# Performance work log

Measured on AMD Instinct MI355X. Metric: run time of the kernel, lower is better.

The kernel has to match this reference:

```python
import jax, jax.numpy as jnp
import numpy as np

G, P = 512, 128            # graphs, nodes per graph
NT, NL, NC = 120, 4, 4     # tracks/leptons/cells per graph (disjoint node targets)
W_NODE, W_BCE, W_F1 = 1.0, 1.0, 1.0  # config['loss weights']


def setup_inputs() -> dict:
    key = jax.random.key(0)
    ks = jax.random.split(key, 8)
    N = G * P
    T, L, C = G * NT, G * NL, G * NC
    E = G * P * P
    local = np.arange(P)[None, :] + (np.arange(G)[:, None] * P)  # [G,P] global node ids
    track_dst = jnp.asarray(local[:, :NT].ravel(), jnp.int32)
    lep_dst = jnp.asarray(local[:, NT:NT + NL].ravel(), jnp.int32)
    cell_dst = jnp.asarray(local[:, NT + NL:].ravel(), jnp.int32)
    ii, jj = np.meshgrid(np.arange(P), np.arange(P), indexing='ij')
    off = (np.arange(G) * P)[:, None, None]
    edge_src = jnp.asarray((off + ii[None]).reshape(-1), jnp.int32)
    edge_dst = jnp.asarray((off + jj[None]).reshape(-1), jnp.int32)
    edge_gid = jnp.asarray(np.repeat(np.arange(G), P * P), jnp.int32)
    node_gid = jnp.asarray(np.repeat(np.arange(G), P), jnp.int32)
    return {
        'node_prediction': jax.random.normal(ks[0], (N, 5), jnp.float32),
        'edge_prediction': jax.random.normal(ks[1], (E,), jnp.float32),
        'ce_weight': jnp.ones((5,), jnp.float32),
        'track_labels': jax.random.randint(ks[2], (T,), 0, 5, jnp.int32),
        'track_vtx': jax.random.randint(ks[3], (T,), 0, 10, jnp.int32),
        'lep_labels': jax.random.randint(ks[4], (L,), 0, 5, jnp.int32),
        'lep_vtx': jax.random.randint(ks[5], (L,), 0, 10, jnp.int32),
        'cell_labels': jax.random.randint(ks[6], (C,), 0, 5, jnp.int32),
        'cell_vtx': jax.random.randint(ks[7], (C,), 0, 10, jnp.int32),
        'track_dst': track_dst,
        'lep_dst': lep_dst,
        'cell_dst': cell_dst,
        'edge_src': edge_src,
        'edge_dst': edge_dst,
        'edge_gid': edge_gid,
        'node_gid': node_gid,
    }


def reference(node_prediction, edge_prediction, ce_weight,
              track_labels, track_vtx, lep_labels, lep_vtx, cell_labels, cell_vtx,
              track_dst, lep_dst, cell_dst, edge_src, edge_dst, edge_gid, node_gid):
    N = node_prediction.shape[0]

    def scatter(track_v, lep_v, cell_v):  # copy_src + sum over 3 edge types
        out = jnp.zeros((N,), jnp.int32)
        out = out.at[track_dst].add(track_v)
        out = out.at[lep_dst].add(lep_v)
        out = out.at[cell_dst].add(cell_v)
        return out

    node_labels = scatter(track_labels, lep_labels, cell_labels)
    node_vtx = scatter(track_vtx, lep_vtx, cell_vtx)

    # node CrossEntropyLoss (weight=[1]*5, ignore_index=-1, reduction='none')
    logp = jax.nn.log_softmax(node_prediction, axis=-1)
    valid = node_labels != -1
    lab = jnp.clip(node_labels, 0, 4)
    ce = -jnp.take_along_axis(logp, lab[:, None], axis=-1)[:, 0] * ce_weight[lab]
    ce = jnp.where(valid, ce, 0.0)
    node_loss = jax.ops.segment_sum(ce, node_gid, num_segments=G).mean()

    # edge weights (EdgeWeightFunction) and labels (EdgeLabelFunction)
    src_lab = node_labels[edge_src]
    dst_lab = node_labels[edge_dst]
    cond = ((dst_lab == 3) | (dst_lab == 2)) & ((src_lab == 3) | (src_lab == 2))
    w = jnp.where(cond, 2.0, 1.0).astype(jnp.float32)
    y = (node_vtx[edge_src] == node_vtx[edge_dst]).astype(jnp.float32)

    x = edge_prediction
    # BCEWithLogits: log(1+e^x) - x*y
    bce = (jnp.logaddexp(0.0, x) - x * y) * w
    e_cnt = jax.ops.segment_sum(jnp.ones_like(x), edge_gid, num_segments=G)
    edge_bce = (jax.ops.segment_sum(bce, edge_gid, num_segments=G) / e_cnt).mean()

    yh = jax.nn.sigmoid(x)
    tp = jax.ops.segment_sum(yh * y * w, edge_gid, num_segments=G)
    fn = jax.ops.segment_sum((1.0 - yh) * y * w, edge_gid, num_segments=G)
    fp = jax.ops.segment_sum(yh * (1.0 - y) * w, edge_gid, num_segments=G)
    edge_f1 = -(2.0 * tp / (2.0 * tp + fp + fn + 1e-10)).mean()

    loss = node_loss * W_NODE + edge_bce * W_BCE + edge_f1 * W_F1
    return loss
```

## Files before the change

kernel.cpp:

```cpp
#include <hip/hip_runtime.h>
#include <math.h>

#define NG     512
#define NP     128
#define NTRK   120
#define NLEP   4
#define NCEL   4
#define EPG    (NP * NP)
#define NTHREADS 1024
#define F4ITERS (EPG / (NTHREADS * 4))

__global__ __launch_bounds__(NTHREADS) void vfl_main(
    const float* __restrict__ node_pred,
    const float* __restrict__ edge_pred,
    const float* __restrict__ ce_weight,
    const int* __restrict__ track_labels, const int* __restrict__ track_vtx,
    const int* __restrict__ lep_labels,   const int* __restrict__ lep_vtx,
    const int* __restrict__ cell_labels,  const int* __restrict__ cell_vtx,
    float* __restrict__ gout)
{
    const int g = blockIdx.x;
    const int t = threadIdx.x;
    const int wv = t >> 6;
    const int ln = t & 63;

    __shared__ float s_edge[EPG];
    __shared__ int   s_pack[NP];
    __shared__ float s_red[16][4];
    __shared__ int   s_cnt[10][2];

    {
        const float* ep_base = edge_pred + (size_t)g * EPG;
        #pragma unroll
        for (int k = 0; k < 4; ++k) {
            const int c = (k << 4) + wv;
            const float* gsrc = ep_base + c * 256 + ln * 4;
            __builtin_amdgcn_global_load_lds(
                (const __attribute__((address_space(1))) void*)gsrc,
                (__attribute__((address_space(3))) void*)&s_edge[c * 256],
                16, 0, 0);
        }
    }

    if (t < 20) ((int*)s_cnt)[t] = 0;

    float ce = 0.0f;
    int vtx = 0, is23 = 0;
    if (t < NP) {
        int lab;
        if (t < NTRK) {
            lab = track_labels[g * NTRK + t];
            vtx = track_vtx  [g * NTRK + t];
        } else if (t < NTRK + NLEP) {
            const int u = t - NTRK;
            lab = lep_labels[g * NLEP + u];
            vtx = lep_vtx  [g * NLEP + u];
        } else {
            const int u = t - NTRK - NLEP;
            lab = cell_labels[g * NCEL + u];
            vtx = cell_vtx  [g * NCEL + u];
        }
        is23 = (lab == 2 || lab == 3) ? 1 : 0;
        s_pack[t] = (vtx & 0xff) | (is23 << 8);

        const float* np = node_pred + (size_t)(g * NP + t) * 5;
        const float x0 = np[0], x1 = np[1], x2 = np[2], x3 = np[3], x4 = np[4];
        const float m  = fmaxf(fmaxf(fmaxf(x0, x1), fmaxf(x2, x3)), x4);
        const float sm = __expf(x0 - m) + __expf(x1 - m) + __expf(x2 - m)
                       + __expf(x3 - m) + __expf(x4 - m);
        const float lse = m + __logf(sm);
        const float xl = (lab == 0) ? x0 : (lab == 1) ? x1 : (lab == 2) ? x2
                       : (lab == 3) ? x3 : x4;
        ce = (lse - xl) * ce_weight[lab];
    }

    asm volatile("s_waitcnt vmcnt(0)" ::: "memory");
    __syncthreads();

    if (t < NP) atomicAdd(&s_cnt[vtx][is23], 1);

    const int j0 = (t & 31) << 2;
    const int pj0 = s_pack[j0 + 0];
    const int pj1 = s_pack[j0 + 1];
    const int pj2 = s_pack[j0 + 2];
    const int pj3 = s_pack[j0 + 3];
    const int ibase = t >> 5;

    const float4* se4 = (const float4*)s_edge;

    float bce = 0.0f, swyh = 0.0f, tp = 0.0f;

    #pragma unroll
    for (int k = 0; k < F4ITERS; ++k) {
        const float4 v  = se4[k * NTHREADS + t];
        const int    pi = s_pack[ibase + k * 32];

        const float xs[4]  = { v.x, v.y, v.z, v.w };
        const int   pjs[4] = { pj0, pj1, pj2, pj3 };
        #pragma unroll
        for (int c = 0; c < 4; ++c) {
            const float x   = xs[c];
            const int   pjc = pjs[c];
            const bool  same = (((pi ^ pjc) & 0xff) == 0);
            const float w   = ((pi & pjc) & 0x100) ? 2.0f : 1.0f;
            const float wf  = same ? w : 0.0f;
            const float e  = __expf(-fabsf(x));
            const float t1 = 1.0f + e;
            const float r  = __builtin_amdgcn_rcpf(t1);
            const float sp = fmaxf(x, 0.0f) + __logf(t1);
            const float yh = (x >= 0.0f) ? r : (1.0f - r);
            bce  = fmaf(w,  sp, bce);
            bce  = fmaf(wf, -x, bce);
            swyh = fmaf(w,  yh, swyh);
            tp   = fmaf(wf, yh, tp);
        }
    }

    float vals[4] = { ce, bce, swyh, tp };
    #pragma unroll
    for (int i = 0; i < 4; ++i) {
        float x = vals[i];
        #pragma unroll
        for (int off = 32; off > 0; off >>= 1)
            x += __shfl_xor(x, off, 64);
        vals[i] = x;
    }
    if (ln == 0) {
        #pragma unroll
        for (int i = 0; i < 4; ++i) s_red[wv][i] = vals[i];
    }
    __syncthreads();

    if (t < 64) {
        float x[4];
        #pragma unroll
        for (int i = 0; i < 4; ++i)
            x[i] = (t < 16) ? s_red[t][i] : 0.0f;
        #pragma unroll
        for (int i = 0; i < 4; ++i) {
            #pragma unroll
            for (int off = 32; off > 0; off >>= 1)
                x[i] += __shfl_xor(x[i], off, 64);
        }
        if (t == 0) {
            int swfy = 0;
            #pragma unroll
            for (int vv = 0; vv < 10; ++vv) {
                const int n0 = s_cnt[vv][0], n1 = s_cnt[vv][1];
                const int nt = n0 + n1;
                swfy += nt * nt + n1 * n1;
            }
            const float gce = x[0], gbce = x[1], gswyh = x[2], gtp = x[3];
            const float fn = (float)swfy - gtp;
            const float fp = gswyh - gtp;
            const float f1 = (2.0f * gtp) / (2.0f * gtp + fp + fn + 1e-10f);
            gout[g] = gce + gbce * (1.0f / (float)EPG) - f1;
        }
    }
}

__global__ __launch_bounds__(256) void vfl_finalize(
    const float* __restrict__ gout, float* __restrict__ out)
{
    const int t = threadIdx.x;
    float acc = gout[t] + gout[t + 256];
    #pragma unroll
    for (int off = 32; off > 0; off >>= 1)
        acc += __shfl_xor(acc, off, 64);
    __shared__ float sred[4];
    if ((t & 63) == 0) sred[t >> 6] = acc;
    __syncthreads();
    if (t == 0)
        out[0] = (sred[0] + sred[1] + sred[2] + sred[3]) * (1.0f / NG);
}

extern "C" void kernel_launch(void* const* d_in, const int* in_sizes, int n_in,
                              void* d_out, int out_size, void* d_ws, size_t ws_size,
                              hipStream_t stream)
{
    const float* node_pred    = (const float*)d_in[0];
    const float* edge_pred    = (const float*)d_in[1];
    const float* ce_weight    = (const float*)d_in[2];
    const int*   track_labels = (const int*)d_in[3];
    const int*   track_vtx    = (const int*)d_in[4];
    const int*   lep_labels   = (const int*)d_in[5];
    const int*   lep_vtx     = (const int*)d_in[6];
    const int*   cell_labels  = (const int*)d_in[7];
    const int*   cell_vtx    = (const int*)d_in[8];

    float* gout = (float*)d_ws;
    float* out  = (float*)d_out;

    vfl_main<<<NG, NTHREADS, 0, stream>>>(
        node_pred, edge_pred, ce_weight,
        track_labels, track_vtx, lep_labels, lep_vtx, cell_labels, cell_vtx,
        gout);
    vfl_finalize<<<1, 256, 0, stream>>>(gout, out);
}
```

Measured before the change: 18.45 us.

## Pipeline per-wave edge chunk loads with incremental vmcnt waits instead of full drain

Each wave now processes only the edge chunks it loaded into LDS itself. The row index is derived from the chunk, so each step can wait with a decreasing vmcnt instead of draining every load behind a block barrier. Node prediction and label loads are issued before the edge loads, and the softmax cross-entropy is computed while the edge loads are in flight. The goal is to overlap the load latency with compute inside a block, at the cost of reliance on in-order vmcnt accounting and explicit scheduling barriers.

```diff
diff --git a/kernel.cpp b/kernel.cpp
--- a/kernel.cpp
+++ b/kernel.cpp
@@ -8,7 +8,7 @@
 #define NCEL   4
 #define EPG    (NP * NP)
 #define NTHREADS 1024
-#define F4ITERS (EPG / (NTHREADS * 4))
+#define NSTEPS 4
 
 __global__ __launch_bounds__(NTHREADS) void vfl_main(
     const float* __restrict__ node_pred,
@@ -29,25 +29,11 @@
     __shared__ float s_red[16][4];
     __shared__ int   s_cnt[10][2];
 
-    {
-        const float* ep_base = edge_pred + (size_t)g * EPG;
-        #pragma unroll
-        for (int k = 0; k < 4; ++k) {
-            const int c = (k << 4) + wv;
-            const float* gsrc = ep_base + c * 256 + ln * 4;
-            __builtin_amdgcn_global_load_lds(
-                (const __attribute__((address_space(1))) void*)gsrc,
-                (__attribute__((address_space(3))) void*)&s_edge[c * 256],
-                16, 0, 0);
-        }
-    }
-
     if (t < 20) ((int*)s_cnt)[t] = 0;
 
-    float ce = 0.0f;
-    int vtx = 0, is23 = 0;
+    float x0 = 0.f, x1 = 0.f, x2 = 0.f, x3 = 0.f, x4 = 0.f, cw = 0.f;
+    int lab = 0, vtx = 0, is23 = 0;
     if (t < NP) {
-        int lab;
         if (t < NTRK) {
             lab = track_labels[g * NTRK + t];
             vtx = track_vtx  [g * NTRK + t];
@@ -64,43 +50,66 @@
         s_pack[t] = (vtx & 0xff) | (is23 << 8);
 
         const float* np = node_pred + (size_t)(g * NP + t) * 5;
-        const float x0 = np[0], x1 = np[1], x2 = np[2], x3 = np[3], x4 = np[4];
+        x0 = np[0]; x1 = np[1]; x2 = np[2]; x3 = np[3]; x4 = np[4];
+        cw = ce_weight[lab];
+    }
+
+    __builtin_amdgcn_sched_barrier(0);
+
+    {
+        const float* ep_base = edge_pred + (size_t)g * EPG;
+        #pragma unroll
+        for (int k = 0; k < NSTEPS; ++k) {
+            const int c = (k << 4) + wv;
+            const float* gsrc = ep_base + c * 256 + ln * 4;
+            __builtin_amdgcn_global_load_lds(
+                (const __attribute__((address_space(1))) void*)gsrc,
+                (__attribute__((address_space(3))) void*)&s_edge[c * 256],
+                16, 0, 0);
+        }
+    }
+    __builtin_amdgcn_sched_barrier(0);
+
+    float ce = 0.0f;
+    if (t < NP) {
         const float m  = fmaxf(fmaxf(fmaxf(x0, x1), fmaxf(x2, x3)), x4);
         const float sm = __expf(x0 - m) + __expf(x1 - m) + __expf(x2 - m)
                        + __expf(x3 - m) + __expf(x4 - m);
         const float lse = m + __logf(sm);
         const float xl = (lab == 0) ? x0 : (lab == 1) ? x1 : (lab == 2) ? x2
                        : (lab == 3) ? x3 : x4;
-        ce = (lse - xl) * ce_weight[lab];
-    }
-
-    asm volatile("s_waitcnt vmcnt(0)" ::: "memory");
-    __syncthreads();
+        ce = (lse - xl) * cw;
+    }
+
+    asm volatile("s_waitcnt lgkmcnt(0)" ::: "memory");
+    __builtin_amdgcn_s_barrier();
+    __builtin_amdgcn_sched_barrier(0);
 
     if (t < NP) atomicAdd(&s_cnt[vtx][is23], 1);
 
-    const int j0 = (t & 31) << 2;
+    const int j0 = (ln & 31) << 2;
     const int pj0 = s_pack[j0 + 0];
     const int pj1 = s_pack[j0 + 1];
     const int pj2 = s_pack[j0 + 2];
     const int pj3 = s_pack[j0 + 3];
-    const int ibase = t >> 5;
-
-    const float4* se4 = (const float4*)s_edge;
 
     float bce = 0.0f, swyh = 0.0f, tp = 0.0f;
 
     #pragma unroll
-    for (int k = 0; k < F4ITERS; ++k) {
-        const float4 v  = se4[k * NTHREADS + t];
-        const int    pi = s_pack[ibase + k * 32];
+    for (int k = 0; k < NSTEPS; ++k) {
+        asm volatile("s_waitcnt vmcnt(%0)" :: "n"(NSTEPS - 1 - k) : "memory");
+        __builtin_amdgcn_sched_barrier(0);
+
+        const int c = (k << 4) + wv;
+        const float4 v  = *(const float4*)&s_edge[c * 256 + (ln << 2)];
+        const int    pi = s_pack[c * 2 + (ln >> 5)];
 
         const float xs[4]  = { v.x, v.y, v.z, v.w };
         const int   pjs[4] = { pj0, pj1, pj2, pj3 };
         #pragma unroll
-        for (int c = 0; c < 4; ++c) {
-            const float x   = xs[c];
-            const int   pjc = pjs[c];
+        for (int cc = 0; cc < 4; ++cc) {
+            const float x   = xs[cc];
+            const int   pjc = pjs[cc];
             const bool  same = (((pi ^ pjc) & 0xff) == 0);
             const float w   = ((pi & pjc) & 0x100) ? 2.0f : 1.0f;
             const float wf  = same ? w : 0.0f;
@@ -184,9 +193,9 @@
     const int*   track_labels = (const int*)d_in[3];
     const int*   track_vtx    = (const int*)d_in[4];
     const int*   lep_labels   = (const int*)d_in[5];
-    const int*   lep_vtx     = (const int*)d_in[6];
+    const int*   lep_vtx      = (const int*)d_in[6];
     const int*   cell_labels  = (const int*)d_in[7];
-    const int*   cell_vtx    = (const int*)d_in[8];
+    const int*   cell_vtx     = (const int*)d_in[8];
 
     float* gout = (float*)d_ws;
     float* out  = (float*)d_out;
```

Measured after the change: 18.39 us. Within noise of the previous version (-0.3%).
